# Performance work log

Hardware: AMD Instinct MI355X
Metric: run time of the kernel (lower is better)

The kernel has to match this reference:

```python
import jax, jax.numpy as jnp
import numpy as np

NUM_HEADS = 4
GROUPS = 16
EPS = 1e-5


def setup_inputs() -> dict:
    key = jax.random.key(0)
    ks = jax.random.split(key, 7)
    b, c, hh, ww = 4, 256, 64, 64
    x = jax.random.normal(ks[0], (b, c, hh, ww), dtype=jnp.float32)
    norm_w = 1.0 + 0.1 * jax.random.normal(ks[1], (c,), dtype=jnp.float32)
    norm_b = 0.1 * jax.random.normal(ks[2], (c,), dtype=jnp.float32)
    qkv_w = jax.random.normal(ks[3], (3 * c, c), dtype=jnp.float32) / np.sqrt(c)
    qkv_b = 0.01 * jax.random.normal(ks[4], (3 * c,), dtype=jnp.float32)
    # NOTE: original zero-inits proj_out; we use random weights so the
    # attention path actually affects the output (kernel correctness test).
    proj_w = jax.random.normal(ks[5], (c, c), dtype=jnp.float32) / np.sqrt(c)
    proj_b = jnp.zeros((c,), dtype=jnp.float32)
    return {"x": x, "norm_w": norm_w, "norm_b": norm_b,
            "qkv_w": qkv_w, "qkv_b": qkv_b,
            "proj_w": proj_w, "proj_b": proj_b}


def _group_norm(x, w, b):
    # x: [B, C, T]; GroupNorm32 computes in fp32 (inputs already fp32)
    B, C, T = x.shape
    xg = x.reshape(B, GROUPS, C // GROUPS, T)
    mean = jnp.mean(xg, axis=(2, 3), keepdims=True)
    var = jnp.var(xg, axis=(2, 3), keepdims=True)
    xn = ((xg - mean) * jax.lax.rsqrt(var + EPS)).reshape(B, C, T)
    return xn * w[None, :, None] + b[None, :, None]


def reference(x, norm_w, norm_b, qkv_w, qkv_b, proj_w, proj_b):
    b, c = x.shape[0], x.shape[1]
    spatial = x.shape[2:]
    x2 = x.reshape(b, c, -1)                       # [B, C, T]
    T = x2.shape[-1]
    normed = _group_norm(x2, norm_w, norm_b)
    qkv = jnp.einsum('oc,bct->bot', qkv_w, normed) + qkv_b[None, :, None]
    # faithful reshape: [B, 3C, T] -> [B*H, 3C/H, T], then split in thirds
    qkv = qkv.reshape(b * NUM_HEADS, (3 * c) // NUM_HEADS, T)
    ch = qkv.shape[1] // 3                         # = C / H
    q, k, v = jnp.split(qkv, 3, axis=1)
    scale = 1.0 / np.sqrt(np.sqrt(ch))
    weight = jnp.einsum('bct,bcs->bts', q * scale, k * scale)
    weight = jax.nn.softmax(weight.astype(jnp.float32), axis=-1).astype(qkv.dtype)
    h = jnp.einsum('bts,bcs->bct', weight, v)      # [B*H, ch, T]
    h = h.reshape(b, c, T)
    h = jnp.einsum('oc,bct->bot', proj_w, h) + proj_b[None, :, None]
    return (x2 + h).reshape(b, c, *spatial)
```

## Files before the change

kernel.cpp:

```cpp
#include <hip/hip_runtime.h>

constexpr int kB  = 4;
constexpr int kC  = 256;
constexpr int kT  = 4096;
constexpr int kG  = 16;
constexpr int kCg = kC / kG;
constexpr int kH  = 4;
constexpr int kCh = kC / kH;
constexpr float kEps = 1e-5f;
constexpr float kQScale = 0.125f * 1.4426950408889634f;

typedef short bf16x8 __attribute__((ext_vector_type(8)));
typedef float f32x4  __attribute__((ext_vector_type(4)));
typedef float f32x16 __attribute__((ext_vector_type(16)));

union PunP { uint4 u; bf16x8 f; };

__device__ inline unsigned short f2bf(float f) {
    union { float f; unsigned u; } v; v.f = f;
    unsigned r = v.u + 0x7fffu + ((v.u >> 16) & 1u);
    return (unsigned short)(r >> 16);
}
__device__ inline unsigned pk2bf(float a, float b) {
    return (unsigned)f2bf(a) | ((unsigned)f2bf(b) << 16);
}
__device__ inline unsigned pk2bf_trunc(float a, float b) {
    return __builtin_amdgcn_perm(__float_as_uint(b), __float_as_uint(a), 0x07060302u);
}
__device__ inline void pls32(unsigned& a, unsigned& b) {
    __asm__("v_permlane32_swap_b32 %0, %1" : "+v"(a), "+v"(b));
}

__global__ __launch_bounds__(256) void prep_kernel(const float* __restrict__ x,
                                                   float* __restrict__ stats,
                                                   const float* __restrict__ qkv_w,
                                                   const float* __restrict__ proj_w,
                                                   unsigned short* __restrict__ wbf) {
    int tid = threadIdx.x;
    if (blockIdx.x >= 256) {
        int gid = (blockIdx.x - 256) * 256 + tid;
        for (int i = gid; i < 65536; i += 128 * 256) {
            float4 v = (i < 49152) ? ((const float4*)qkv_w)[i]
                                   : ((const float4*)proj_w)[i - 49152];
            *(uint2*)&wbf[(size_t)i * 4] = make_uint2(pk2bf(v.x, v.y), pk2bf(v.z, v.w));
        }
        return;
    }
    int bg = blockIdx.x >> 2, part = blockIdx.x & 3;
    const float4* xp4 = (const float4*)(x + (size_t)bg * (kCg * kT)) + part * 4096;
    float s = 0.f, q = 0.f;
    #pragma unroll 4
    for (int i = 0; i < 16; ++i) {
        float4 v = xp4[tid + i * 256];
        s += v.x + v.y + v.z + v.w;
        q += v.x * v.x + v.y * v.y + v.z * v.z + v.w * v.w;
    }
    #pragma unroll
    for (int off = 32; off > 0; off >>= 1) {
        s += __shfl_down(s, off);
        q += __shfl_down(q, off);
    }
    __shared__ float rs[4], rq[4];
    int wid = tid >> 6, lane = tid & 63;
    if (lane == 0) { rs[wid] = s; rq[wid] = q; }
    __syncthreads();
    if (tid == 0) {
        float S = rs[0] + rs[1] + rs[2] + rs[3];
        float Q = rq[0] + rq[1] + rq[2] + rq[3];
        stats[blockIdx.x * 2 + 0] = S;
        stats[blockIdx.x * 2 + 1] = Q;
    }
}

__global__ __launch_bounds__(256) void gn_apply_t_kernel(const float* __restrict__ x,
                                                         const float* __restrict__ stats,
                                                         const float* __restrict__ w,
                                                         const float* __restrict__ bias,
                                                         unsigned short* __restrict__ normT) {
    __shared__ float Ls[64][65];
    int t0 = blockIdx.x * 64;
    int c0 = blockIdx.y * 64;
    int b  = blockIdx.z;
    int tid = threadIdx.x;
    const float invN = 1.0f / (float)(kCg * kT);
    #pragma unroll
    for (int p = 0; p < 4; ++p) {
        int idx = tid + p * 256;
        int cl = idx >> 4, t4 = idx & 15;
        int c = c0 + cl;
        int bg = b * kG + (c >> 4);
        float S = 0.f, Q = 0.f;
        #pragma unroll
        for (int pr = 0; pr < 4; ++pr) {
            S += stats[(bg * 4 + pr) * 2 + 0];
            Q += stats[(bg * 4 + pr) * 2 + 1];
        }
        float mean = S * invN;
        float rstd = rsqrtf(Q * invN - mean * mean + kEps);
        float sw = w[c] * rstd;
        float sb = bias[c] - mean * sw;
        float4 v = *(const float4*)&x[((size_t)b * kC + c) * kT + t0 + t4 * 4];
        Ls[t4 * 4 + 0][cl] = v.x * sw + sb;
        Ls[t4 * 4 + 1][cl] = v.y * sw + sb;
        Ls[t4 * 4 + 2][cl] = v.z * sw + sb;
        Ls[t4 * 4 + 3][cl] = v.w * sw + sb;
    }
    __syncthreads();
    {
        int row = tid >> 2, cq = (tid & 3) * 16;
        unsigned tmp[8];
        #pragma unroll
        for (int i = 0; i < 8; ++i)
            tmp[i] = pk2bf(Ls[row][cq + 2 * i], Ls[row][cq + 2 * i + 1]);
        uint4* dst = (uint4*)&normT[((size_t)b * kT + t0 + row) * kC + c0 + cq];
        dst[0] = make_uint4(tmp[0], tmp[1], tmp[2], tmp[3]);
        dst[1] = make_uint4(tmp[4], tmp[5], tmp[6], tmp[7]);
    }
}

__global__ __launch_bounds__(256) void qkv_gemm_kernel(const unsigned short* __restrict__ wbf,
                                                       const float* __restrict__ qkv_b,
                                                       const unsigned short* __restrict__ normT,
                                                       unsigned short* __restrict__ qTg,
                                                       unsigned short* __restrict__ kTg,
                                                       unsigned short* __restrict__ vCg) {
    constexpr int LDK = 72;
    constexpr int LDV = 264;
    __shared__ __align__(16) unsigned short As[64 * LDK];
    __shared__ __align__(16) unsigned short Bs[256 * LDK];

    int t0 = blockIdx.x * 256;
    int m0 = blockIdx.y * 64;
    int b  = blockIdx.z;
    const unsigned short* Ab = wbf + (size_t)m0 * kC;
    const unsigned short* Bb = normT + (size_t)b * kT * kC;

    int tid = threadIdx.x;
    int wave = tid >> 6, lane = tid & 63;
    int ln15 = lane & 15, quad = lane >> 4;
    int wm = wave >> 1, wt = wave & 1;

    f32x4 acc[2][8] = {};

    for (int k0 = 0; k0 < kC; k0 += 64) {
        __syncthreads();
        #pragma unroll
        for (int p = 0; p < 2; ++p) {
            int idx = tid + p * 256;
            int row = idx >> 3, seg = idx & 7;
            *(uint4*)&As[row * LDK + seg * 8] =
                *(const uint4*)&Ab[(size_t)row * kC + k0 + seg * 8];
        }
        #pragma unroll
        for (int p = 0; p < 8; ++p) {
            int idx = tid + p * 256;
            int row = idx >> 3, seg = idx & 7;
            *(uint4*)&Bs[row * LDK + seg * 8] =
                *(const uint4*)&Bb[(size_t)(t0 + row) * kC + k0 + seg * 8];
        }
        __syncthreads();
        #pragma unroll
        for (int ks = 0; ks < 2; ++ks) {
            bf16x8 af[2], bf[8];
            #pragma unroll
            for (int i = 0; i < 2; ++i)
                af[i] = *(bf16x8*)&As[(wm * 32 + i * 16 + ln15) * LDK + ks * 32 + quad * 8];
            #pragma unroll
            for (int j = 0; j < 8; ++j)
                bf[j] = *(bf16x8*)&Bs[(wt * 128 + j * 16 + ln15) * LDK + ks * 32 + quad * 8];
            #pragma unroll
            for (int i = 0; i < 2; ++i)
                #pragma unroll
                for (int j = 0; j < 8; ++j)
                    acc[i][j] = __builtin_amdgcn_mfma_f32_16x16x32_bf16(
                        af[i], bf[j], acc[i][j], 0, 0, 0);
        }
    }

    int type = (m0 % 192) / 64;
    int h = m0 / 192;
    int bh = b * kH + h;
    __syncthreads();
    #pragma unroll
    for (int i = 0; i < 2; ++i) {
        float4 bv = *(const float4*)&qkv_b[m0 + wm * 32 + i * 16 + quad * 4];
        const float* bp = (const float*)&bv;
        #pragma unroll
        for (int j = 0; j < 8; ++j) {
            int tl = wt * 128 + j * 16 + ln15;
            int c = wm * 32 + i * 16 + quad * 4;
            float v0 = acc[i][j][0] + bp[0];
            float v1 = acc[i][j][1] + bp[1];
            float v2 = acc[i][j][2] + bp[2];
            float v3 = acc[i][j][3] + bp[3];
            if (type == 0) {
                v0 *= kQScale; v1 *= kQScale; v2 *= kQScale; v3 *= kQScale;
            }
            if (type != 2) {
                *(uint2*)&Bs[tl * LDK + c] = make_uint2(pk2bf(v0, v1), pk2bf(v2, v3));
            } else {
                Bs[(c + 0) * LDV + tl] = f2bf(v0);
                Bs[(c + 1) * LDV + tl] = f2bf(v1);
                Bs[(c + 2) * LDV + tl] = f2bf(v2);
                Bs[(c + 3) * LDV + tl] = f2bf(v3);
            }
        }
    }
    __syncthreads();
    if (type != 2) {
        unsigned short* base = ((type == 0) ? qTg : kTg) + (size_t)bh * (kT * kCh);
        #pragma unroll
        for (int p = 0; p < 8; ++p) {
            int f = tid + p * 256;
            int ln = f & 31, hif = (f >> 5) & 1, ks = (f >> 6) & 3, tb = f >> 8;
            *(uint4*)&base[((t0 >> 5) + tb) * 2048 + ks * 512 + hif * 256 + ln * 8] =
                *(uint4*)&Bs[(tb * 32 + ln) * LDK + ks * 16 + hif * 8];
        }
    } else {
        unsigned short* base = vCg + (size_t)bh * (kT * kCh);
        #pragma unroll
        for (int p = 0; p < 8; ++p) {
            int f = tid + p * 256;
            int c = f & 63, hif = (f >> 6) & 1, sg = f >> 7;
            *(uint4*)&base[((t0 >> 4) + sg) * 1024 + hif * 512 + c * 8] =
                *(uint4*)&Bs[c * LDV + sg * 16 + hif * 8];
        }
    }
}

__global__ __launch_bounds__(256, 2) void attn_mfma_kernel(const unsigned short* __restrict__ qTg,
                                                           const unsigned short* __restrict__ kTg,
                                                           const unsigned short* __restrict__ vCg,
                                                           unsigned short* __restrict__ attnT) {
    __shared__ float Ored[2][2][32][64];
    __shared__ float Lred[2][2][64];

    int lid = blockIdx.y * 32 + blockIdx.x;
    int wl  = (lid & 7) * 64 + (lid >> 3);
    int bh  = wl >> 5;
    int t0  = (wl & 31) * 128;
    int b = bh >> 2, h = bh & 3;

    int tid = threadIdx.x;
    int wave = tid >> 6, lane = tid & 63;
    int ln31 = lane & 31, hi = lane >> 5;
    int tc = wave & 1;
    int sh = wave >> 1;

    const unsigned short* qb = qTg + (size_t)bh * (kT * kCh);
    const unsigned short* kb = kTg + (size_t)bh * (kT * kCh);
    const unsigned short* vb = vCg + (size_t)bh * (kT * kCh);

    bf16x8 qA[4], qB[4];
    {
        const unsigned short* qp = qb + ((size_t)(t0 >> 5) + tc * 2) * 2048 + hi * 256 + ln31 * 8;
        #pragma unroll
        for (int ks = 0; ks < 4; ++ks) {
            qA[ks] = *(const bf16x8*)(qp + ks * 512);
            qB[ks] = *(const bf16x8*)(qp + 2048 + ks * 512);
        }
    }

    const unsigned short* kbase = kb + (size_t)sh * 131072 + hi * 256 + ln31 * 8;
    const unsigned short* vbase = vb + (size_t)sh * 131072 + hi * 512 + ln31 * 8;

    float lA = 0.f, lB = 0.f;
    f32x16 oA0 = {}, oA1 = {}, oB0 = {}, oB1 = {};

    auto loadKV = [&](bf16x8* kf, bf16x8* vf, int idx) {
        const unsigned short* kp = kbase + (size_t)idx * 2048;
        const unsigned short* vp = vbase + (size_t)idx * 2048;
        kf[0] = *(const bf16x8*)(kp);
        kf[1] = *(const bf16x8*)(kp + 512);
        kf[2] = *(const bf16x8*)(kp + 1024);
        kf[3] = *(const bf16x8*)(kp + 1536);
        vf[0] = *(const bf16x8*)(vp);
        vf[1] = *(const bf16x8*)(vp + 256);
        vf[2] = *(const bf16x8*)(vp + 1024);
        vf[3] = *(const bf16x8*)(vp + 1280);
    };

    auto softmax_pack = [&](const f32x16& s, float& l, bf16x8& f0, bf16x8& f1) {
        unsigned u00, u01, u10, u11, u20, u21, u30, u31;
        {
            float p0 = __builtin_amdgcn_exp2f(s[0]);
            float p1 = __builtin_amdgcn_exp2f(s[1]);
            float p2 = __builtin_amdgcn_exp2f(s[2]);
            float p3 = __builtin_amdgcn_exp2f(s[3]);
            l += (p0 + p1) + (p2 + p3);
            u00 = pk2bf_trunc(p0, p1); u01 = pk2bf_trunc(p2, p3);
        }
        {
            float p0 = __builtin_amdgcn_exp2f(s[4]);
            float p1 = __builtin_amdgcn_exp2f(s[5]);
            float p2 = __builtin_amdgcn_exp2f(s[6]);
            float p3 = __builtin_amdgcn_exp2f(s[7]);
            l += (p0 + p1) + (p2 + p3);
            u10 = pk2bf_trunc(p0, p1); u11 = pk2bf_trunc(p2, p3);
        }
        {
            float p0 = __builtin_amdgcn_exp2f(s[8]);
            float p1 = __builtin_amdgcn_exp2f(s[9]);
            float p2 = __builtin_amdgcn_exp2f(s[10]);
            float p3 = __builtin_amdgcn_exp2f(s[11]);
            l += (p0 + p1) + (p2 + p3);
            u20 = pk2bf_trunc(p0, p1); u21 = pk2bf_trunc(p2, p3);
        }
        {
            float p0 = __builtin_amdgcn_exp2f(s[12]);
            float p1 = __builtin_amdgcn_exp2f(s[13]);
            float p2 = __builtin_amdgcn_exp2f(s[14]);
            float p3 = __builtin_amdgcn_exp2f(s[15]);
            l += (p0 + p1) + (p2 + p3);
            u30 = pk2bf_trunc(p0, p1); u31 = pk2bf_trunc(p2, p3);
        }
        pls32(u00, u10); pls32(u01, u11);
        pls32(u20, u30); pls32(u21, u31);
        PunP P0, P1;
        P0.u = make_uint4(u00, u01, u10, u11);
        P1.u = make_uint4(u20, u21, u30, u31);
        f0 = P0.f; f1 = P1.f;
    };

    auto computeTile = [&](const bf16x8* kf, const bf16x8* vf) {
        f32x16 sA = {}, sB = {};
        __builtin_amdgcn_s_setprio(1);
        #pragma unroll
        for (int ks = 0; ks < 4; ++ks) {
            sA = __builtin_amdgcn_mfma_f32_32x32x16_bf16(kf[ks], qA[ks], sA, 0, 0, 0);
            sB = __builtin_amdgcn_mfma_f32_32x32x16_bf16(kf[ks], qB[ks], sB, 0, 0, 0);
        }
        __builtin_amdgcn_s_setprio(0);
        bf16x8 FA0, FA1, FB0, FB1;
        softmax_pack(sA, lA, FA0, FA1);
        softmax_pack(sB, lB, FB0, FB1);
        __builtin_amdgcn_s_setprio(1);
        oA0 = __builtin_amdgcn_mfma_f32_32x32x16_bf16(vf[0], FA0, oA0, 0, 0, 0);
        oA1 = __builtin_amdgcn_mfma_f32_32x32x16_bf16(vf[1], FA0, oA1, 0, 0, 0);
        oB0 = __builtin_amdgcn_mfma_f32_32x32x16_bf16(vf[0], FB0, oB0, 0, 0, 0);
        oB1 = __builtin_amdgcn_mfma_f32_32x32x16_bf16(vf[1], FB0, oB1, 0, 0, 0);
        oA0 = __builtin_amdgcn_mfma_f32_32x32x16_bf16(vf[2], FA1, oA0, 0, 0, 0);
        oA1 = __builtin_amdgcn_mfma_f32_32x32x16_bf16(vf[3], FA1, oA1, 0, 0, 0);
        oB0 = __builtin_amdgcn_mfma_f32_32x32x16_bf16(vf[2], FB1, oB0, 0, 0, 0);
        oB1 = __builtin_amdgcn_mfma_f32_32x32x16_bf16(vf[3], FB1, oB1, 0, 0, 0);
        __builtin_amdgcn_s_setprio(0);
    };

    bf16x8 kX[4], vX[4], kY[4], vY[4];
    loadKV(kX, vX, 0);
    __builtin_amdgcn_sched_barrier(0);
    #pragma unroll 1
    for (int it = 0; it < 64; it += 2) {
        loadKV(kY, vY, it + 1);
        __builtin_amdgcn_sched_barrier(0);
        computeTile(kX, vX);
        loadKV(kX, vX, (it + 2) & 63);
        __builtin_amdgcn_sched_barrier(0);
        computeTile(kY, vY);
    }

    lA += __shfl_xor(lA, 32);
    lB += __shfl_xor(lB, 32);

    if (sh == 1) {
        #pragma unroll
        for (int e = 0; e < 16; ++e) {
            Ored[tc][0][e][lane]      = oA0[e];
            Ored[tc][0][16 + e][lane] = oA1[e];
            Ored[tc][1][e][lane]      = oB0[e];
            Ored[tc][1][16 + e][lane] = oB1[e];
        }
        Lred[tc][0][lane] = lA;
        Lred[tc][1][lane] = lB;
    }
    __syncthreads();
    if (sh == 0) {
        #pragma unroll
        for (int e = 0; e < 16; ++e) {
            oA0[e] += Ored[tc][0][e][lane];
            oA1[e] += Ored[tc][0][16 + e][lane];
            oB0[e] += Ored[tc][1][e][lane];
            oB1[e] += Ored[tc][1][16 + e][lane];
        }
        lA += Lred[tc][0][lane];
        lB += Lred[tc][1][lane];
        #pragma unroll
        for (int ch = 0; ch < 2; ++ch) {
            float linv = 1.0f / (ch ? lB : lA);
            int t = t0 + tc * 64 + ch * 32 + ln31;
            #pragma unroll
            for (int ct = 0; ct < 2; ++ct) {
                const f32x16& ao = ch ? (ct ? oB1 : oB0) : (ct ? oA1 : oA0);
                #pragma unroll
                for (int g = 0; g < 4; ++g) {
                    int c = h * kCh + ct * 32 + 8 * g + 4 * hi;
                    float v0 = ao[4 * g + 0] * linv;
                    float v1 = ao[4 * g + 1] * linv;
                    float v2 = ao[4 * g + 2] * linv;
                    float v3 = ao[4 * g + 3] * linv;
                    *(uint2*)&attnT[((size_t)b * kT + t) * kC + c] =
                        make_uint2(pk2bf(v0, v1), pk2bf(v2, v3));
                }
            }
        }
    }
}

__global__ __launch_bounds__(256) void proj_gemm_kernel(const unsigned short* __restrict__ wpbf,
                                                        const float* __restrict__ proj_b,
                                                        const unsigned short* __restrict__ attnT,
                                                        const float* __restrict__ x,
                                                        float* __restrict__ out) {
    constexpr int LDK = 72;
    __shared__ __align__(16) unsigned short As[64 * LDK];
    __shared__ __align__(16) unsigned short Bs[256 * LDK];

    int t0 = blockIdx.x * 256;
    int m0 = blockIdx.y * 64;
    int b  = blockIdx.z;
    const unsigned short* Ab = wpbf + (size_t)m0 * kC;
    const unsigned short* Bb = attnT + (size_t)b * kT * kC;

    int tid = threadIdx.x;
    int wave = tid >> 6, lane = tid & 63;
    int ln15 = lane & 15, quad = lane >> 4;
    int wm = wave >> 1, wt = wave & 1;

    f32x4 acc[2][8] = {};

    for (int k0 = 0; k0 < kC; k0 += 64) {
        __syncthreads();
        #pragma unroll
        for (int p = 0; p < 2; ++p) {
            int idx = tid + p * 256;
            int row = idx >> 3, seg = idx & 7;
            *(uint4*)&As[row * LDK + seg * 8] =
                *(const uint4*)&Ab[(size_t)row * kC + k0 + seg * 8];
        }
        #pragma unroll
        for (int p = 0; p < 8; ++p) {
            int idx = tid + p * 256;
            int row = idx >> 3, seg = idx & 7;
            *(uint4*)&Bs[row * LDK + seg * 8] =
                *(const uint4*)&Bb[(size_t)(t0 + row) * kC + k0 + seg * 8];
        }
        __syncthreads();
        #pragma unroll
        for (int ks = 0; ks < 2; ++ks) {
            bf16x8 af[2], bf[8];
            #pragma unroll
            for (int i = 0; i < 2; ++i)
                af[i] = *(bf16x8*)&As[(wm * 32 + i * 16 + ln15) * LDK + ks * 32 + quad * 8];
            #pragma unroll
            for (int j = 0; j < 8; ++j)
                bf[j] = *(bf16x8*)&Bs[(wt * 128 + j * 16 + ln15) * LDK + ks * 32 + quad * 8];
            #pragma unroll
            for (int i = 0; i < 2; ++i)
                #pragma unroll
                for (int j = 0; j < 8; ++j)
                    acc[i][j] = __builtin_amdgcn_mfma_f32_16x16x32_bf16(
                        af[i], bf[j], acc[i][j], 0, 0, 0);
        }
    }

    #pragma unroll
    for (int i = 0; i < 2; ++i) {
        float4 bv = *(const float4*)&proj_b[m0 + wm * 32 + i * 16 + quad * 4];
        const float* bp = (const float*)&bv;
        #pragma unroll
        for (int j = 0; j < 8; ++j) {
            int t = t0 + wt * 128 + j * 16 + ln15;
            int mbase = m0 + wm * 32 + i * 16 + quad * 4;
            #pragma unroll
            for (int r = 0; r < 4; ++r) {
                size_t off = ((size_t)b * kC + mbase + r) * kT + t;
                out[off] = acc[i][j][r] + bp[r] + x[off];
            }
        }
    }
}

extern "C" void kernel_launch(void* const* d_in, const int* in_sizes, int n_in,
                              void* d_out, int out_size, void* d_ws, size_t ws_size,
                              hipStream_t stream) {
    const float* x      = (const float*)d_in[0];
    const float* norm_w = (const float*)d_in[1];
    const float* norm_b = (const float*)d_in[2];
    const float* qkv_w  = (const float*)d_in[3];
    const float* qkv_b  = (const float*)d_in[4];
    const float* proj_w = (const float*)d_in[5];
    const float* proj_b = (const float*)d_in[6];
    float* out = (float*)d_out;

    float* stats = (float*)d_ws;
    unsigned short* wsbf  = (unsigned short*)((float*)d_ws + 512);
    unsigned short* normT = wsbf;
    unsigned short* wbf   = normT + (size_t)kB * kT * kC;
    unsigned short* qTp   = wbf + 262144;
    unsigned short* kTp   = qTp + (size_t)kB * kH * kT * kCh;
    unsigned short* vCp   = kTp + (size_t)kB * kH * kT * kCh;
    unsigned short* attnT = vCp + (size_t)kB * kH * kT * kCh;
    unsigned short* wpbf  = wbf + 196608;

    prep_kernel<<<384, 256, 0, stream>>>(x, stats, qkv_w, proj_w, wbf);
    gn_apply_t_kernel<<<dim3(kT / 64, kC / 64, kB), 256, 0, stream>>>(
        x, stats, norm_w, norm_b, normT);
    qkv_gemm_kernel<<<dim3(kT / 256, 12, kB), 256, 0, stream>>>(
        wbf, qkv_b, normT, qTp, kTp, vCp);
    attn_mfma_kernel<<<dim3(kT / 128, kB * kH), 256, 0, stream>>>(qTp, kTp, vCp, attnT);
    proj_gemm_kernel<<<dim3(kT / 256, kC / 64, kB), 256, 0, stream>>>(
        wpbf, proj_b, attnT, x, out);
}
```

Measured before the change: 184.0 us.

## Fuse GroupNorm stats and apply into one cooperative kernel with grid sync

Merges the stats/weight-conversion prep kernel and the normalize-transpose kernel into a single cooperative launch. Each block loads its x tile once into registers, writes partial sums per group, does a grid-wide sync, then reduces the group stats and applies normalization from the held registers. This drops one kernel launch and the second full read of x. In exchange it needs all 1024 blocks co-resident for the grid barrier and pays the cost of that barrier.

Result: slower. 244.5 us (+32.9%).

```diff
diff --git a/kernel.cpp b/kernel.cpp
--- a/kernel.cpp
+++ b/kernel.cpp
@@ -1,4 +1,7 @@
 #include <hip/hip_runtime.h>
+#include <hip/hip_cooperative_groups.h>
+
+namespace cg = cooperative_groups;
 
 constexpr int kB  = 4;
 constexpr int kC  = 256;
@@ -31,79 +34,91 @@
     __asm__("v_permlane32_swap_b32 %0, %1" : "+v"(a), "+v"(b));
 }
 
-__global__ __launch_bounds__(256) void prep_kernel(const float* __restrict__ x,
-                                                   float* __restrict__ stats,
-                                                   const float* __restrict__ qkv_w,
-                                                   const float* __restrict__ proj_w,
-                                                   unsigned short* __restrict__ wbf) {
+__global__ __launch_bounds__(256) void gn_fused_kernel(const float* __restrict__ x,
+                                                       float* __restrict__ stats,
+                                                       const float* __restrict__ qkv_w,
+                                                       const float* __restrict__ proj_w,
+                                                       unsigned short* __restrict__ wbf,
+                                                       const float* __restrict__ w,
+                                                       const float* __restrict__ bias,
+                                                       unsigned short* __restrict__ normT) {
+    __shared__ float Ls[64][65];
+    __shared__ float rS[4][4], rQ[4][4];
+    __shared__ float gS[4], gQ[4];
+
+    int bx = blockIdx.x, by = blockIdx.y, bz = blockIdx.z;
+    int t0 = bx * 64, c0 = by * 64, b = bz;
     int tid = threadIdx.x;
-    if (blockIdx.x >= 256) {
-        int gid = (blockIdx.x - 256) * 256 + tid;
-        for (int i = gid; i < 65536; i += 128 * 256) {
-            float4 v = (i < 49152) ? ((const float4*)qkv_w)[i]
-                                   : ((const float4*)proj_w)[i - 49152];
-            *(uint2*)&wbf[(size_t)i * 4] = make_uint2(pk2bf(v.x, v.y), pk2bf(v.z, v.w));
-        }
-        return;
-    }
-    int bg = blockIdx.x >> 2, part = blockIdx.x & 3;
-    const float4* xp4 = (const float4*)(x + (size_t)bg * (kCg * kT)) + part * 4096;
-    float s = 0.f, q = 0.f;
-    #pragma unroll 4
-    for (int i = 0; i < 16; ++i) {
-        float4 v = xp4[tid + i * 256];
-        s += v.x + v.y + v.z + v.w;
-        q += v.x * v.x + v.y * v.y + v.z * v.z + v.w * v.w;
+    int wid = tid >> 6, lane = tid & 63;
+    int lid = bx + 64 * (by + 4 * bz);
+
+    if (tid < 64) {
+        int i = lid * 64 + tid;
+        float4 v = (i < 49152) ? ((const float4*)qkv_w)[i]
+                               : ((const float4*)proj_w)[i - 49152];
+        *(uint2*)&wbf[(size_t)i * 4] = make_uint2(pk2bf(v.x, v.y), pk2bf(v.z, v.w));
+    }
+
+    float4 xv[4];
+    float s[4], q[4];
+    #pragma unroll
+    for (int p = 0; p < 4; ++p) {
+        int idx = tid + p * 256;
+        int cl = idx >> 4, t4 = idx & 15;
+        xv[p] = *(const float4*)&x[((size_t)b * kC + c0 + cl) * kT + t0 + t4 * 4];
+        s[p] = (xv[p].x + xv[p].y) + (xv[p].z + xv[p].w);
+        q[p] = (xv[p].x * xv[p].x + xv[p].y * xv[p].y)
+             + (xv[p].z * xv[p].z + xv[p].w * xv[p].w);
     }
     #pragma unroll
     for (int off = 32; off > 0; off >>= 1) {
-        s += __shfl_down(s, off);
-        q += __shfl_down(q, off);
-    }
-    __shared__ float rs[4], rq[4];
-    int wid = tid >> 6, lane = tid & 63;
-    if (lane == 0) { rs[wid] = s; rq[wid] = q; }
+        #pragma unroll
+        for (int p = 0; p < 4; ++p) {
+            s[p] += __shfl_down(s[p], off);
+            q[p] += __shfl_down(q[p], off);
+        }
+    }
+    if (lane == 0) {
+        #pragma unroll
+        for (int p = 0; p < 4; ++p) { rS[wid][p] = s[p]; rQ[wid][p] = q[p]; }
+    }
     __syncthreads();
-    if (tid == 0) {
-        float S = rs[0] + rs[1] + rs[2] + rs[3];
-        float Q = rq[0] + rq[1] + rq[2] + rq[3];
-        stats[blockIdx.x * 2 + 0] = S;
-        stats[blockIdx.x * 2 + 1] = Q;
-    }
-}
-
-__global__ __launch_bounds__(256) void gn_apply_t_kernel(const float* __restrict__ x,
-                                                         const float* __restrict__ stats,
-                                                         const float* __restrict__ w,
-                                                         const float* __restrict__ bias,
-                                                         unsigned short* __restrict__ normT) {
-    __shared__ float Ls[64][65];
-    int t0 = blockIdx.x * 64;
-    int c0 = blockIdx.y * 64;
-    int b  = blockIdx.z;
-    int tid = threadIdx.x;
+    if (tid < 4) {
+        float S = rS[0][tid] + rS[1][tid] + rS[2][tid] + rS[3][tid];
+        float Q = rQ[0][tid] + rQ[1][tid] + rQ[2][tid] + rQ[3][tid];
+        int grp = bz * 16 + by * 4 + tid;
+        stats[(grp * 64 + bx) * 2 + 0] = S;
+        stats[(grp * 64 + bx) * 2 + 1] = Q;
+    }
+
+    cg::this_grid().sync();
+
+    {
+        int grp = bz * 16 + by * 4 + wid;
+        float S = stats[(grp * 64 + lane) * 2 + 0];
+        float Q = stats[(grp * 64 + lane) * 2 + 1];
+        #pragma unroll
+        for (int off = 32; off > 0; off >>= 1) {
+            S += __shfl_down(S, off);
+            Q += __shfl_down(Q, off);
+        }
+        if (lane == 0) { gS[wid] = S; gQ[wid] = Q; }
+    }
+    __syncthreads();
     const float invN = 1.0f / (float)(kCg * kT);
     #pragma unroll
     for (int p = 0; p < 4; ++p) {
         int idx = tid + p * 256;
         int cl = idx >> 4, t4 = idx & 15;
         int c = c0 + cl;
-        int bg = b * kG + (c >> 4);
-        float S = 0.f, Q = 0.f;
-        #pragma unroll
-        for (int pr = 0; pr < 4; ++pr) {
-            S += stats[(bg * 4 + pr) * 2 + 0];
-            Q += stats[(bg * 4 + pr) * 2 + 1];
-        }
-        float mean = S * invN;
-        float rstd = rsqrtf(Q * invN - mean * mean + kEps);
+        float mean = gS[p] * invN;
+        float rstd = rsqrtf(gQ[p] * invN - mean * mean + kEps);
         float sw = w[c] * rstd;
         float sb = bias[c] - mean * sw;
-        float4 v = *(const float4*)&x[((size_t)b * kC + c) * kT + t0 + t4 * 4];
-        Ls[t4 * 4 + 0][cl] = v.x * sw + sb;
-        Ls[t4 * 4 + 1][cl] = v.y * sw + sb;
-        Ls[t4 * 4 + 2][cl] = v.z * sw + sb;
-        Ls[t4 * 4 + 3][cl] = v.w * sw + sb;
+        Ls[t4 * 4 + 0][cl] = xv[p].x * sw + sb;
+        Ls[t4 * 4 + 1][cl] = xv[p].y * sw + sb;
+        Ls[t4 * 4 + 2][cl] = xv[p].z * sw + sb;
+        Ls[t4 * 4 + 3][cl] = xv[p].w * sw + sb;
     }
     __syncthreads();
     {
@@ -493,7 +508,7 @@
     float* out = (float*)d_out;
 
     float* stats = (float*)d_ws;
-    unsigned short* wsbf  = (unsigned short*)((float*)d_ws + 512);
+    unsigned short* wsbf  = (unsigned short*)((float*)d_ws + 8192);
     unsigned short* normT = wsbf;
     unsigned short* wbf   = normT + (size_t)kB * kT * kC;
     unsigned short* qTp   = wbf + 262144;
@@ -502,9 +517,10 @@
     unsigned short* attnT = vCp + (size_t)kB * kH * kT * kCh;
     unsigned short* wpbf  = wbf + 196608;
 
-    prep_kernel<<<384, 256, 0, stream>>>(x, stats, qkv_w, proj_w, wbf);
-    gn_apply_t_kernel<<<dim3(kT / 64, kC / 64, kB), 256, 0, stream>>>(
-        x, stats, norm_w, norm_b, normT);
+    void* gn_args[] = { (void*)&x, (void*)&stats, (void*)&qkv_w, (void*)&proj_w,
+                        (void*)&wbf, (void*)&norm_w, (void*)&norm_b, (void*)&normT };
+    hipLaunchCooperativeKernel((const void*)gn_fused_kernel, dim3(kT / 64, kC / 64, kB),
+                               dim3(256, 1, 1), gn_args, 0, stream);
     qkv_gemm_kernel<<<dim3(kT / 256, 12, kB), 256, 0, stream>>>(
         wbf, qkv_b, normT, qTp, kTp, vCp);
     attn_mfma_kernel<<<dim3(kT / 128, kB * kH), 256, 0, stream>>>(qTp, kTp, vCp, attnT);
```
